# Performance work log

Hardware: AMD Instinct MI355X
Metric: run time of the kernel (lower is better)

Reference implementation:

```python
import jax, jax.numpy as jnp
import numpy as np

ALPHA = 0.2          # LeakyReLU negative slope
NEG_INF = -9e15      # masking value from the original module


def setup_inputs() -> dict:
    key = jax.random.key(0)
    kw, ka, k1, k2, k3 = jax.random.split(key, 5)
    B, N1, N2, F, O = 4, 2048, 2048, 256, 256
    word = jax.random.normal(kw, (B, N2, F), dtype=jnp.float32)
    # 0/1 hypergraph incidence matrix (float, as in the torch module)
    adj = jax.random.randint(ka, (B, N1, N2), 0, 2).astype(jnp.float32)
    stdv = 1.0 / np.sqrt(O)
    W1 = jax.random.uniform(k1, (F, O), jnp.float32, -stdv, stdv)
    W2 = jax.random.uniform(k2, (F, O), jnp.float32, -stdv, stdv)
    w3 = jax.random.uniform(k3, (2 * O, 1), jnp.float32, -stdv, stdv)
    return {"word": word, "adj": adj, "W1": W1, "W2": W2, "w3": w3}


def reference(word, adj, W1, W2, w3):
    # word: [B, N2, F]; adj: [B, N1, N2]; W1/W2: [F, O]; w3: [2O, 1]
    O = W1.shape[1]
    # mean-pool neighbor features per hyperedge (row-normalized adj)
    deg = jnp.sum(adj, axis=-1, keepdims=True)                 # [B, N1, 1]
    deg = jnp.where(deg > 0, deg, jnp.ones_like(deg))
    mp = jnp.matmul(adj / deg, word)                           # [B, N1, F]
    # The original builds 4D tensors h1[b,i,j,:] = adj[b,i,j]*word[b,j,:] and
    # h_mp[b,i,j,:] = adj[b,i,j]*mp[b,i,:], projects both and dots with w3.
    # Since scaling commutes with the linear maps, the scalar score is
    #   adj[b,i,j] * (word[b,j] @ W1 @ w3_a + mp[b,i] @ W2 @ w3_b)
    w3a = w3[:O, 0]                                            # pairs with w1h
    w3b = w3[O:, 0]                                            # pairs with w2h
    s1 = jnp.einsum('bnf,fo,o->bn', word, W1, w3a)             # [B, N2]
    s2 = jnp.einsum('bnf,fo,o->bn', mp, W2, w3b)               # [B, N1]
    pre = adj * (s2[:, :, None] + s1[:, None, :])              # [B, N1, N2]
    alpha = jnp.exp(jax.nn.leaky_relu(pre, ALPHA))
    attention = jnp.where(adj > 0, alpha, NEG_INF)
    attention_edge = jax.nn.softmax(attention, axis=2)         # over N2
    edge = jnp.matmul(attention_edge, word)                    # [B, N1, F]
    return edge
```

## Files before the change

kernel.cpp:

```cpp
#include <hip/hip_runtime.h>

#define B 4
#define N 2048
#define F 256
#define O 256
#define LOG2E 1.4426950408889634f
#define NEG_BIG -9000000000000000.0f

typedef _Float16 f16;
typedef f16 f16x8 __attribute__((ext_vector_type(8)));
typedef float f32x16 __attribute__((ext_vector_type(16)));

#define WS_V1 0
#define WS_V2 256
#define WS_T1 512
#define WS_T2 (512 + B*N)
#define WS_S2 (512 + 2*B*N)
#define WS_CR (512 + 3*B*N)
#define WS_WN (512 + 4*B*N)
#define WT_OFF (1u << 20)
#define MK_OFF (6u << 20)

__device__ __forceinline__ float alpha_of(float pre2) {
  return __builtin_amdgcn_exp2f(fmaxf(pre2, 0.2f * pre2));
}

__global__ __launch_bounds__(256) void k_v(const float* __restrict__ W1,
                                           const float* __restrict__ W2,
                                           const float* __restrict__ w3,
                                           float* __restrict__ ws) {
  int tid = threadIdx.x;
  int lane = tid & 63;
  int f = blockIdx.x * 4 + (tid >> 6);
  float a = 0.f, b = 0.f;
  #pragma unroll
  for (int k = 0; k < 4; ++k) {
    int o = lane + 64 * k;
    a += W1[f * O + o] * w3[o];
    b += W2[f * O + o] * w3[O + o];
  }
  #pragma unroll
  for (int off = 32; off > 0; off >>= 1) {
    a += __shfl_down(a, off);
    b += __shfl_down(b, off);
  }
  if (lane == 0) {
    ws[WS_V1 + f] = a;
    ws[WS_V2 + f] = b;
  }
}

__global__ __launch_bounds__(256) void k_prep(const float* __restrict__ word,
                                              float* __restrict__ ws,
                                              f16* __restrict__ wordT) {
  __shared__ float v1s[F], v2s[F];
  __shared__ __align__(16) f16 tile[F][40];
  int t = threadIdx.x;
  int k0 = blockIdx.x * 32;
  int b = blockIdx.y;

  if (t < 64)       ((float4*)v1s)[t]      = ((const float4*)(ws + WS_V1))[t];
  else if (t < 128) ((float4*)v2s)[t - 64] = ((const float4*)(ws + WS_V2))[t - 64];
  __syncthreads();

  int r = t >> 3;
  int cg = t & 7;
  const float* wrow = word + ((size_t)(b * N + k0 + r)) * F;
  float a = 0.f, bb = 0.f;
  #pragma unroll
  for (int i = 0; i < 8; ++i) {
    int c = i * 32 + cg * 4;
    float4 w = *(const float4*)(wrow + c);
    float4 x1 = *(const float4*)(v1s + c);
    float4 x2 = *(const float4*)(v2s + c);
    a  += w.x * x1.x + w.y * x1.y + w.z * x1.z + w.w * x1.w;
    bb += w.x * x2.x + w.y * x2.y + w.z * x2.z + w.w * x2.w;
    tile[c + 0][r] = (f16)w.x;
    tile[c + 1][r] = (f16)w.y;
    tile[c + 2][r] = (f16)w.z;
    tile[c + 3][r] = (f16)w.w;
  }
  #pragma unroll
  for (int off = 4; off > 0; off >>= 1) {
    a  += __shfl_down(a, off);
    bb += __shfl_down(bb, off);
  }
  if (cg == 0) {
    ws[WS_T1 + b * N + k0 + r] = a * LOG2E;
    ws[WS_T2 + b * N + k0 + r] = bb;
  }
  __syncthreads();

  size_t base = (size_t)b * F * N;
  #pragma unroll
  for (int i = 0; i < 4; ++i) {
    int idx = t + 256 * i;
    int ft = idx >> 7, c = (idx >> 6) & 1, l = idx & 63;
    int f = ft * 32 + (l & 31);
    int rr = c * 16 + ((l >> 5) * 8);
    f16x8 h = *(const f16x8*)&tile[f][rr];
    *(f16x8*)(wordT + base + ((size_t)((ft * 128 + (k0 >> 4) + c) * 64 + l)) * 8) = h;
  }
}

__global__ __launch_bounds__(256) void k_stats(const float* __restrict__ adj,
                                               float* __restrict__ ws,
                                               unsigned char* __restrict__ mask) {
  int row = blockIdx.x;
  int b = row >> 11;
  int t = threadIdx.x;
  int wid = t >> 6, lane = t & 63;
  const float* arow = adj + (size_t)row * N;
  const float* t1b = ws + WS_T1 + b * N;
  const float* t2b = ws + WS_T2 + b * N;

  float4 a0 = *(const float4*)(arow + t * 8);
  float4 a1 = *(const float4*)(arow + t * 8 + 4);
  float4 u0 = *(const float4*)(t2b + t * 8);
  float4 u1 = *(const float4*)(t2b + t * 8 + 4);
  float deg = a0.x + a0.y + a0.z + a0.w + a1.x + a1.y + a1.z + a1.w;
  float dot = a0.x * u0.x + a0.y * u0.y + a0.z * u0.z + a0.w * u0.w +
              a1.x * u1.x + a1.y * u1.y + a1.z * u1.z + a1.w * u1.w;
  unsigned mb = (a0.x > 0.f ? 1u : 0u) | (a0.y > 0.f ? 2u : 0u) |
                (a0.z > 0.f ? 4u : 0u) | (a0.w > 0.f ? 8u : 0u) |
                (a1.x > 0.f ? 16u : 0u) | (a1.y > 0.f ? 32u : 0u) |
                (a1.z > 0.f ? 64u : 0u) | (a1.w > 0.f ? 128u : 0u);
  mask[(size_t)row * 256 + t] = (unsigned char)mb;

  #pragma unroll
  for (int off = 32; off > 0; off >>= 1) {
    deg += __shfl_down(deg, off);
    dot += __shfl_down(dot, off);
  }
  __shared__ float rd[4], rt[4], rm[4], rz[4];
  if (lane == 0) { rd[wid] = deg; rt[wid] = dot; }
  __syncthreads();
  deg = rd[0] + rd[1] + rd[2] + rd[3];
  dot = rt[0] + rt[1] + rt[2] + rt[3];
  float degc = deg > 0.f ? deg : 1.f;
  float s2p = (dot / degc) * LOG2E;

  float4 p0 = *(const float4*)(t1b + t * 8);
  float4 p1 = *(const float4*)(t1b + t * 8 + 4);
  float al[8];
  al[0] = (mb & 1)   ? alpha_of(p0.x + s2p) : NEG_BIG;
  al[1] = (mb & 2)   ? alpha_of(p0.y + s2p) : NEG_BIG;
  al[2] = (mb & 4)   ? alpha_of(p0.z + s2p) : NEG_BIG;
  al[3] = (mb & 8)   ? alpha_of(p0.w + s2p) : NEG_BIG;
  al[4] = (mb & 16)  ? alpha_of(p1.x + s2p) : NEG_BIG;
  al[5] = (mb & 32)  ? alpha_of(p1.y + s2p) : NEG_BIG;
  al[6] = (mb & 64)  ? alpha_of(p1.z + s2p) : NEG_BIG;
  al[7] = (mb & 128) ? alpha_of(p1.w + s2p) : NEG_BIG;
  float m = NEG_BIG;
  #pragma unroll
  for (int j = 0; j < 8; ++j) m = fmaxf(m, al[j]);
  #pragma unroll
  for (int off = 32; off > 0; off >>= 1) m = fmaxf(m, __shfl_down(m, off));
  if (lane == 0) rm[wid] = m;
  __syncthreads();
  m = fmaxf(fmaxf(rm[0], rm[1]), fmaxf(rm[2], rm[3]));

  float negmL = -m * LOG2E;
  float z = 0.f;
  #pragma unroll
  for (int j = 0; j < 8; ++j) z += __builtin_amdgcn_exp2f(fmaf(al[j], LOG2E, negmL));
  #pragma unroll
  for (int off = 32; off > 0; off >>= 1) z += __shfl_down(z, off);
  if (lane == 0) rz[wid] = z;
  __syncthreads();
  if (t == 0) {
    z = rz[0] + rz[1] + rz[2] + rz[3];
    ws[WS_S2 + row] = s2p;
    if (deg > 0.f) {
      ws[WS_CR + row] = negmL - log2f(z);
      ws[WS_WN + row] = 0.f;
    } else {
      ws[WS_CR + row] = 0.f;
      ws[WS_WN + row] = 1.0f / (float)N;
    }
  }
}

__global__ __launch_bounds__(512, 1) void k_gemm(const f16* __restrict__ wordT,
                                                 const unsigned char* __restrict__ maskg,
                                                 const float* __restrict__ ws,
                                                 float* __restrict__ out) {
  __shared__ __align__(16) f16 Aw[2][2][8][512];
  __shared__ __align__(16) float t1S[N];
  __shared__ float sSC[192];

  const int t = threadIdx.x;
  const int rb = blockIdx.x >> 1, fh = blockIdx.x & 1;
  const int row0 = rb * 64;
  const int b = row0 >> 11;

  *(float4*)&t1S[t * 4] = *(const float4*)(ws + WS_T1 + b * N + t * 4);
  if (t < 64) {
    sSC[t]       = ws[WS_S2 + row0 + t];
    sSC[64 + t]  = ws[WS_CR + row0 + t];
    sSC[128 + t] = ws[WS_WN + row0 + t];
  }
  __syncthreads();

  const int gl = t & 63;
  const int gc = (t >> 6) & 3;
  const int rh_g = t >> 8;
  const int koff = (gl >> 5) * 8;
  const int rowL = rh_g * 32 + (gl & 31);
  const float rs2 = sSC[rowL], rcr = sSC[64 + rowL], rwn = sSC[128 + rowL];
  const unsigned* mrow = (const unsigned*)(maskg + (size_t)(row0 + rowL) * 256);

  const int lw = t & 63;
  const int wv = t >> 6;
  const int rh = wv >> 2;
  const int ftile = fh * 4 + (wv & 3);
  const int fcol = ftile * 32 + (lw & 31);
  const f16* wtb = wordT + (size_t)b * F * N;

  f32x16 acc = {0.f,0.f,0.f,0.f,0.f,0.f,0.f,0.f,0.f,0.f,0.f,0.f,0.f,0.f,0.f,0.f};

  #define GENW(IT, BUF, MW)                                                    \
    {                                                                          \
      const int kb = (IT) * 128 + gc * 32 + koff;                              \
      const float4 ta0 = *(const float4*)&t1S[kb];                             \
      const float4 ta1 = *(const float4*)&t1S[kb + 4];                         \
      const float4 tb0 = *(const float4*)&t1S[kb + 16];                        \
      const float4 tb1 = *(const float4*)&t1S[kb + 20];                        \
      const float ta[8] = {ta0.x, ta0.y, ta0.z, ta0.w, ta1.x, ta1.y, ta1.z, ta1.w}; \
      const float tb[8] = {tb0.x, tb0.y, tb0.z, tb0.w, tb1.x, tb1.y, tb1.z, tb1.w}; \
      const unsigned m0 = (MW) >> koff;                                        \
      const unsigned m1 = (MW) >> (16 + koff);                                 \
      f16x8 h0, h1;                                                            \
      _Pragma("unroll")                                                        \
      for (int j = 0; j < 8; ++j) {                                            \
        float p0 = ta[j] + rs2;                                                \
        float a0v = __builtin_amdgcn_exp2f(fmaxf(p0, 0.2f * p0));              \
        float w0 = ((m0 >> j) & 1u) ? __builtin_amdgcn_exp2f(fmaf(a0v, LOG2E, rcr)) : rwn; \
        h0[j] = (f16)w0;                                                       \
        float p1 = tb[j] + rs2;                                                \
        float a1v = __builtin_amdgcn_exp2f(fmaxf(p1, 0.2f * p1));              \
        float w1 = ((m1 >> j) & 1u) ? __builtin_amdgcn_exp2f(fmaf(a1v, LOG2E, rcr)) : rwn; \
        h1[j] = (f16)w1;                                                       \
      }                                                                        \
      *(f16x8*)&Aw[BUF][rh_g][gc * 2][gl * 8]     = h0;                        \
      *(f16x8*)&Aw[BUF][rh_g][gc * 2 + 1][gl * 8] = h1;                        \
    }

  {
    unsigned mw0 = mrow[gc];
    GENW(0, 0, mw0)
  }
  __syncthreads();

  for (int it = 0; it < 16; ++it) {
    const int cur = it & 1;
    const f16* bp = wtb + ((size_t)(ftile * 128 + it * 8) * 64 + lw) * 8;
    f16x8 bf[8];
    #pragma unroll
    for (int c = 0; c < 8; ++c) bf[c] = *(const f16x8*)(bp + (size_t)c * 512);

    if (it < 15) {
      unsigned mwn = mrow[(it + 1) * 4 + gc];
      GENW(it + 1, cur ^ 1, mwn)
    }

    #pragma unroll
    for (int c = 0; c < 8; ++c) {
      const f16x8 af = *(const f16x8*)&Aw[cur][rh][c][lw * 8];
      acc = __builtin_amdgcn_mfma_f32_32x32x16_f16(af, bf[c], acc, 0, 0, 0);
    }
    __syncthreads();
  }

  #pragma unroll
  for (int reg = 0; reg < 16; ++reg) {
    int lr = rh * 32 + (reg & 3) + 8 * (reg >> 2) + 4 * (lw >> 5);
    out[(size_t)(row0 + lr) * F + fcol] = acc[reg];
  }
}

extern "C" void kernel_launch(void* const* d_in, const int* in_sizes, int n_in,
                              void* d_out, int out_size, void* d_ws, size_t ws_size,
                              hipStream_t stream) {
  const float* word = (const float*)d_in[0];
  const float* adj  = (const float*)d_in[1];
  const float* W1   = (const float*)d_in[2];
  const float* W2   = (const float*)d_in[3];
  const float* w3   = (const float*)d_in[4];
  float* out = (float*)d_out;
  float* ws  = (float*)d_ws;
  f16* wordT = (f16*)((char*)d_ws + WT_OFF);
  unsigned char* mask = (unsigned char*)d_ws + MK_OFF;

  k_v<<<64, 256, 0, stream>>>(W1, W2, w3, ws);
  k_prep<<<dim3(N / 32, B), 256, 0, stream>>>(word, ws, wordT);
  k_stats<<<B * N, 256, 0, stream>>>(adj, ws, mask);
  k_gemm<<<(B * N) / 64 * 2, 512, 0, stream>>>(wordT, mask, ws, out);
}
```

Before: 132.5 us.

## Shrink gemm blocks to 32 rows and software-prefetch next B fragments

Blocks in k_gemm now cover 32 rows with 256 threads instead of 64 rows with 512, and launch bounds allow two blocks per CU, so the grid doubles. The B (wordT) fragments for the next iteration are loaded into registers one iteration ahead, so global load latency overlaps the current MFMAs. The trade-off is more register pressure and twice as many loads of the t1 row and of B tiles across blocks, since B is no longer shared between two row halves.

```diff
diff --git a/kernel.cpp b/kernel.cpp
--- a/kernel.cpp
+++ b/kernel.cpp
@@ -181,39 +181,38 @@
   }
 }
 
-__global__ __launch_bounds__(512, 1) void k_gemm(const f16* __restrict__ wordT,
+__global__ __launch_bounds__(256, 2) void k_gemm(const f16* __restrict__ wordT,
                                                  const unsigned char* __restrict__ maskg,
                                                  const float* __restrict__ ws,
                                                  float* __restrict__ out) {
-  __shared__ __align__(16) f16 Aw[2][2][8][512];
+  __shared__ __align__(16) f16 Aw[2][8][512];
   __shared__ __align__(16) float t1S[N];
-  __shared__ float sSC[192];
+  __shared__ float sSC[96];
 
   const int t = threadIdx.x;
   const int rb = blockIdx.x >> 1, fh = blockIdx.x & 1;
-  const int row0 = rb * 64;
+  const int row0 = rb * 32;
   const int b = row0 >> 11;
 
-  *(float4*)&t1S[t * 4] = *(const float4*)(ws + WS_T1 + b * N + t * 4);
-  if (t < 64) {
-    sSC[t]       = ws[WS_S2 + row0 + t];
-    sSC[64 + t]  = ws[WS_CR + row0 + t];
-    sSC[128 + t] = ws[WS_WN + row0 + t];
+  *(float4*)&t1S[t * 8]     = *(const float4*)(ws + WS_T1 + b * N + t * 8);
+  *(float4*)&t1S[t * 8 + 4] = *(const float4*)(ws + WS_T1 + b * N + t * 8 + 4);
+  if (t < 32) {
+    sSC[t]      = ws[WS_S2 + row0 + t];
+    sSC[32 + t] = ws[WS_CR + row0 + t];
+    sSC[64 + t] = ws[WS_WN + row0 + t];
   }
   __syncthreads();
 
   const int gl = t & 63;
-  const int gc = (t >> 6) & 3;
-  const int rh_g = t >> 8;
+  const int gp = t >> 6;
   const int koff = (gl >> 5) * 8;
-  const int rowL = rh_g * 32 + (gl & 31);
-  const float rs2 = sSC[rowL], rcr = sSC[64 + rowL], rwn = sSC[128 + rowL];
+  const int rowL = gl & 31;
+  const float rs2 = sSC[rowL], rcr = sSC[32 + rowL], rwn = sSC[64 + rowL];
   const unsigned* mrow = (const unsigned*)(maskg + (size_t)(row0 + rowL) * 256);
 
   const int lw = t & 63;
   const int wv = t >> 6;
-  const int rh = wv >> 2;
-  const int ftile = fh * 4 + (wv & 3);
+  const int ftile = fh * 4 + wv;
   const int fcol = ftile * 32 + (lw & 31);
   const f16* wtb = wordT + (size_t)b * F * N;
 
@@ -221,7 +220,7 @@
 
   #define GENW(IT, BUF, MW)                                                    \
     {                                                                          \
-      const int kb = (IT) * 128 + gc * 32 + koff;                              \
+      const int kb = (IT) * 128 + gp * 32 + koff;                              \
       const float4 ta0 = *(const float4*)&t1S[kb];                             \
       const float4 ta1 = *(const float4*)&t1S[kb + 4];                         \
       const float4 tb0 = *(const float4*)&t1S[kb + 16];                        \
@@ -242,39 +241,50 @@
         float w1 = ((m1 >> j) & 1u) ? __builtin_amdgcn_exp2f(fmaf(a1v, LOG2E, rcr)) : rwn; \
         h1[j] = (f16)w1;                                                       \
       }                                                                        \
-      *(f16x8*)&Aw[BUF][rh_g][gc * 2][gl * 8]     = h0;                        \
-      *(f16x8*)&Aw[BUF][rh_g][gc * 2 + 1][gl * 8] = h1;                        \
-    }
-
+      *(f16x8*)&Aw[BUF][gp * 2][gl * 8]     = h0;                              \
+      *(f16x8*)&Aw[BUF][gp * 2 + 1][gl * 8] = h1;                              \
+    }
+
+  f16x8 bf[8];
   {
-    unsigned mw0 = mrow[gc];
+    const f16* bp = wtb + ((size_t)(ftile * 128) * 64 + lw) * 8;
+    #pragma unroll
+    for (int c = 0; c < 8; ++c) bf[c] = *(const f16x8*)(bp + (size_t)c * 512);
+  }
+  {
+    unsigned mw0 = mrow[gp];
     GENW(0, 0, mw0)
   }
   __syncthreads();
 
+  #pragma unroll 2
   for (int it = 0; it < 16; ++it) {
     const int cur = it & 1;
-    const f16* bp = wtb + ((size_t)(ftile * 128 + it * 8) * 64 + lw) * 8;
-    f16x8 bf[8];
-    #pragma unroll
-    for (int c = 0; c < 8; ++c) bf[c] = *(const f16x8*)(bp + (size_t)c * 512);
-
+    f16x8 bfn[8];
     if (it < 15) {
-      unsigned mwn = mrow[(it + 1) * 4 + gc];
+      const f16* bp = wtb + ((size_t)(ftile * 128 + (it + 1) * 8) * 64 + lw) * 8;
+      #pragma unroll
+      for (int c = 0; c < 8; ++c) bfn[c] = *(const f16x8*)(bp + (size_t)c * 512);
+      unsigned mwn = mrow[(it + 1) * 4 + gp];
       GENW(it + 1, cur ^ 1, mwn)
     }
 
     #pragma unroll
     for (int c = 0; c < 8; ++c) {
-      const f16x8 af = *(const f16x8*)&Aw[cur][rh][c][lw * 8];
+      const f16x8 af = *(const f16x8*)&Aw[cur][c][lw * 8];
       acc = __builtin_amdgcn_mfma_f32_32x32x16_f16(af, bf[c], acc, 0, 0, 0);
     }
     __syncthreads();
+
+    if (it < 15) {
+      #pragma unroll
+      for (int c = 0; c < 8; ++c) bf[c] = bfn[c];
+    }
   }
 
   #pragma unroll
   for (int reg = 0; reg < 16; ++reg) {
-    int lr = rh * 32 + (reg & 3) + 8 * (reg >> 2) + 4 * (lw >> 5);
+    int lr = (reg & 3) + 8 * (reg >> 2) + 4 * (lw >> 5);
     out[(size_t)(row0 + lr) * F + fcol] = acc[reg];
   }
 }
@@ -295,5 +305,5 @@
   k_v<<<64, 256, 0, stream>>>(W1, W2, w3, ws);
   k_prep<<<dim3(N / 32, B), 256, 0, stream>>>(word, ws, wordT);
   k_stats<<<B * N, 256, 0, stream>>>(adj, ws, mask);
-  k_gemm<<<(B * N) / 64 * 2, 512, 0, stream>>>(wordT, mask, ws, out);
-}
+  k_gemm<<<(B * N) / 32 * 2, 256, 0, stream>>>(wordT, mask, ws, out);
+}
```

Result: no change. 131.9 us (-0.4%).
